# Performance work log

Measured on AMD Instinct MI355X. Metric: run time of the kernel, lower is better.

Reference implementation:

```python
import jax, jax.numpy as jnp
import numpy as np
import math

NUM_BITS = 8
EPS = 1e-5


def fake_quant(x, num_bits=NUM_BITS):
    """Uniform fake quantization over the tensor's full range (min/max), STE-friendly."""
    qmax = 2.0 ** num_bits - 1.0
    mn = jnp.min(x)
    mx = jnp.max(x)
    scale = jnp.maximum((mx - mn) / qmax, 1e-8)
    q = jnp.round(jnp.clip((x - mn) / scale, 0.0, qmax)) * scale + mn
    # straight-through estimator: forward = q, backward = identity
    return x + jax.lax.stop_gradient(q - x)


def qconv(x, w, stride, pad):
    """QConv2d: fake-quantize input (8b) and weight (8b), then fp conv (no bias)."""
    return jax.lax.conv_general_dilated(
        fake_quant(x), fake_quant(w),
        window_strides=(stride, stride),
        padding=[(pad, pad), (pad, pad)],
        dimension_numbers=("NCHW", "OIHW", "NCHW"))


def range_norm(x, gamma, beta):
    """RangeN / RangeBN (Banner et al.): per-channel mean subtraction and
    range-based scale (max-min over N,H,W) with the Gaussian range correction
    factor; affine params with 8-bit fake-quantized gamma."""
    B, C, H, W = x.shape
    n = B * H * W  # elements per channel
    scale_fix = (0.5 * 0.35) * (1.0 + (math.pi * math.log(4.0)) ** 0.5) / ((2.0 * math.log(n)) ** 0.5)
    mean = jnp.mean(x, axis=(0, 2, 3), keepdims=True)          # [1,C,1,1]
    xc = x - mean
    rng = jnp.max(xc, axis=(0, 2, 3), keepdims=True) - jnp.min(xc, axis=(0, 2, 3), keepdims=True)
    out = xc / (rng * scale_fix + EPS)
    qg = fake_quant(gamma)
    return out * qg[None, :, None, None] + beta[None, :, None, None]


def qsum(a, b):
    """Qsum: fake-quantize both addends to 8 bits, then add."""
    return fake_quant(a) + fake_quant(b)


def setup_inputs() -> dict:
    key = jax.random.key(0)
    ks = jax.random.split(key, 4)
    B, Cin, H, W = 64, 1024, 14, 14
    P = 256  # planes; expansion 4 -> Cout = 1024 == Cin (identity residual)
    x = jax.random.normal(ks[0], (B, Cin, H, W), jnp.float32)
    w1 = jax.random.normal(ks[1], (P, Cin, 1, 1), jnp.float32) * (1.0 / math.sqrt(Cin))
    w2 = jax.random.normal(ks[2], (P, P, 3, 3), jnp.float32) * (1.0 / math.sqrt(P * 9))
    w3 = jax.random.normal(ks[3], (4 * P, P, 1, 1), jnp.float32) * (1.0 / math.sqrt(P))
    g1 = jnp.ones((P,), jnp.float32); b1 = jnp.zeros((P,), jnp.float32)
    g2 = jnp.ones((P,), jnp.float32); b2 = jnp.zeros((P,), jnp.float32)
    g3 = jnp.ones((4 * P,), jnp.float32); b3 = jnp.zeros((4 * P,), jnp.float32)
    return {"x": x, "w1": w1, "g1": g1, "b1": b1, "w2": w2, "g2": g2, "b2": b2,
            "w3": w3, "g3": g3, "b3": b3}


def reference(x, w1, g1, b1, w2, g2, b2, w3, g3, b3):
    out = qconv(x, w1, stride=1, pad=0)
    out = range_norm(out, g1, b1)
    out = qconv(out, w2, stride=1, pad=1)
    out = range_norm(out, g2, b2)
    out = qconv(out, w3, stride=1, pad=0)
    out = range_norm(out, g3, b3)
    return qsum(x, out)  # downsample is None -> identity residual
```

## Files before the change

kernel.cpp:

```cpp
#include <hip/hip_runtime.h>
#include <math.h>

#ifndef M_PI
#define M_PI 3.14159265358979323846
#endif

#define NB   64
#define NCOL 12544

typedef __attribute__((ext_vector_type(4))) int int4v;

static const size_t OF_OUT = 0;
static const size_t OF_XC  = 3211264;
static const size_t OF_Z1P = 6422528;
static const size_t OF_Z2C = 7471104;
static const size_t OF_WQ1 = 8273920;
static const size_t OF_WQ2 = 8339456;
static const size_t OF_WQ3 = 8486912;
static const size_t OF_R1  = 8552448;
static const size_t OF_R2  = 8552704;
static const size_t OF_R3  = 8552960;
static const size_t OF_T2  = 8553984;
static const size_t OF_CX  = 8556032;
static const size_t OF_U2  = 8568576;
static const size_t OF_CZ  = 8597504;
static const size_t OF_SD1 = 8610048;
static const size_t OF_SD2 = 8610560;
static const size_t OF_SD3 = 8611072;
static const size_t OF_MN1 = 8613120;
static const size_t OF_MX1 = 8613376;
static const size_t OF_MN2 = 8613632;
static const size_t OF_MX2 = 8613888;
static const size_t OF_MN3 = 8614144;
static const size_t OF_MX3 = 8615168;
static const size_t OF_PMM = 9061632;
static const size_t OF_ST  = 9068800;

__device__ __forceinline__ float fqv(float v, float mn, float sc) {
    float t = (v - mn) / sc;
    t = fminf(fmaxf(t, 0.0f), 255.0f);
    return rintf(t) * sc + mn;
}
__device__ __forceinline__ float codef(float v, float mn, float sc) {
    float t = (v - mn) / sc;
    t = fminf(fmaxf(t, 0.0f), 255.0f);
    return rintf(t) - 128.0f;
}
__device__ __forceinline__ unsigned short f2bf(float f) { return (unsigned short)(__float_as_uint(f) >> 16); }
__device__ __forceinline__ float bf2f(unsigned short u) { return __uint_as_float(((unsigned)u) << 16); }
__device__ __forceinline__ int pack4(float a, float b, float c, float d) {
    return (int)(unsigned char)(signed char)(int)a | ((int)(unsigned char)(signed char)(int)b << 8) |
           ((int)(unsigned char)(signed char)(int)c << 16) | ((int)(unsigned char)(signed char)(int)d << 24);
}
__device__ __forceinline__ void glds16(const void* g, void* l) {
    __builtin_amdgcn_global_load_lds((const __attribute__((address_space(1))) unsigned int*)g,
                                     (__attribute__((address_space(3))) unsigned int*)l, 16, 0, 0);
}
__device__ __forceinline__ unsigned fkey(float f) {
    unsigned u = __float_as_uint(f);
    return (u & 0x80000000u) ? ~u : (u | 0x80000000u);
}
__device__ __forceinline__ float unfkey(unsigned k) {
    unsigned u = (k & 0x80000000u) ? (k & 0x7FFFFFFFu) : ~k;
    return __uint_as_float(u);
}

__device__ __forceinline__ void blk_minmax(float& mn, float& mx, volatile float* scr) {
    for (int o = 32; o; o >>= 1) {
        mn = fminf(mn, __shfl_down(mn, o, 64));
        mx = fmaxf(mx, __shfl_down(mx, o, 64));
    }
    int lane = threadIdx.x & 63, wv = threadIdx.x >> 6;
    __syncthreads();
    if (lane == 0) { scr[wv] = mn; scr[4 + wv] = mx; }
    __syncthreads();
    mn = fminf(fminf(scr[0], scr[1]), fminf(scr[2], scr[3]));
    mx = fmaxf(fmaxf(scr[4], scr[5]), fmaxf(scr[6], scr[7]));
}

template <int C>
__device__ void stage_params(const float* __restrict__ gamma, const float* __restrict__ beta,
                             const double* __restrict__ sumd, const unsigned* __restrict__ mnk,
                             const unsigned* __restrict__ mxk, float scale_fix,
                             float* lmean, float* lsg, volatile float* scr,
                             float& zmn, float& zsc) {
    int t = threadIdx.x;
    float gmn = INFINITY, gmx = -INFINITY;
    for (int c = t; c < C; c += 256) {
        float g = gamma[c];
        gmn = fminf(gmn, g); gmx = fmaxf(gmx, g);
    }
    blk_minmax(gmn, gmx, scr);
    float gsc = fmaxf((gmx - gmn) / 255.0f, 1e-8f);
    float qmn = INFINITY, qmx = -INFINITY;
    for (int c = t; c < C; c += 256) {
        float mean = (float)sumd[c] / 12544.0f;
        float cmn = unfkey(mnk[c]), cmx = unfkey(mxk[c]);
        float rng = cmx - cmn;
        float qg = fqv(gamma[c], gmn, gsc);
        float s = qg / (rng * scale_fix + 1e-5f);
        if (lmean) { lmean[c] = mean; lsg[c] = s; }
        float b = beta[c];
        float lo = (cmn - mean) * s + b;
        float hi = (cmx - mean) * s + b;
        qmn = fminf(qmn, fminf(lo, hi));
        qmx = fmaxf(qmx, fmaxf(lo, hi));
    }
    blk_minmax(qmn, qmx, scr);
    zmn = qmn;
    zsc = fmaxf((qmx - qmn) / 255.0f, 1e-8f);
}

__global__ __launch_bounds__(256) void k_minmax_all(const float4* __restrict__ x, const float4* __restrict__ w1,
                                                    const float4* __restrict__ w2, const float4* __restrict__ w3,
                                                    float* __restrict__ Pmm, float* __restrict__ Wf) {
    {
        unsigned g = blockIdx.x * 256 + threadIdx.x;
        int* zp = (int*)(Wf + OF_Z1P);
        for (unsigned i = g; i < 1048576u; i += 327680u) zp[i] = 0;
        if (g < 12544u) Wf[OF_CX + g] = 0.0f;
        if (g < 16384u) Wf[OF_U2 + g] = 0.0f;
        if (g < 3072u)  ((int*)(Wf + OF_SD1))[g] = 0;
        if (g < 256u) {
            ((unsigned*)(Wf + OF_MN1))[g] = 0xFF800000u;
            ((unsigned*)(Wf + OF_MX1))[g] = 0x007FFFFFu;
            ((unsigned*)(Wf + OF_MN2))[g] = 0xFF800000u;
            ((unsigned*)(Wf + OF_MX2))[g] = 0x007FFFFFu;
        }
        if (g < 1024u) {
            ((unsigned*)(Wf + OF_MN3))[g] = 0xFF800000u;
            ((unsigned*)(Wf + OF_MX3))[g] = 0x007FFFFFu;
        }
    }
    int b = blockIdx.x;
    const float4* p; int lb, nb, n4, base;
    if (b < 1024)      { p = x;  lb = b;        nb = 1024; n4 = 3211264; base = 0; }
    else if (b < 1088) { p = w1; lb = b - 1024; nb = 64;   n4 = 65536;   base = 2048; }
    else if (b < 1216) { p = w2; lb = b - 1088; nb = 128;  n4 = 147456;  base = 2176; }
    else               { p = w3; lb = b - 1216; nb = 64;   n4 = 65536;   base = 2432; }
    float mn = INFINITY, mx = -INFINITY;
    for (int i = lb * 256 + threadIdx.x; i < n4; i += nb * 256) {
        float4 v = p[i];
        mn = fminf(mn, fminf(fminf(v.x, v.y), fminf(v.z, v.w)));
        mx = fmaxf(mx, fmaxf(fmaxf(v.x, v.y), fmaxf(v.z, v.w)));
    }
    for (int o = 32; o; o >>= 1) {
        mn = fminf(mn, __shfl_down(mn, o, 64));
        mx = fmaxf(mx, __shfl_down(mx, o, 64));
    }
    __shared__ float smn[4], smx[4];
    int lane = threadIdx.x & 63, w = threadIdx.x >> 6;
    if (lane == 0) { smn[w] = mn; smx[w] = mx; }
    __syncthreads();
    if (threadIdx.x == 0) {
        for (int i = 1; i < 4; i++) { mn = fminf(mn, smn[i]); mx = fmaxf(mx, smx[i]); }
        Pmm[base + lb * 2]     = mn;
        Pmm[base + lb * 2 + 1] = mx;
    }
}

__global__ __launch_bounds__(256) void k_fqparams2(const float* __restrict__ Pmm, float* __restrict__ sf) {
    __shared__ float sa[4], sb[4];
    int t = threadIdx.x, lane = t & 63, w = t >> 6;
    const int nbs[4]   = {1024, 64, 128, 64};
    const int bases[4] = {0, 2048, 2176, 2432};
    for (int ten = 0; ten < 4; ten++) {
        float mn = INFINITY, mx = -INFINITY;
        for (int i = t; i < nbs[ten]; i += 256) {
            mn = fminf(mn, Pmm[bases[ten] + 2 * i]);
            mx = fmaxf(mx, Pmm[bases[ten] + 2 * i + 1]);
        }
        for (int o = 32; o; o >>= 1) {
            mn = fminf(mn, __shfl_down(mn, o, 64));
            mx = fmaxf(mx, __shfl_down(mx, o, 64));
        }
        if (lane == 0) { sa[w] = mn; sb[w] = mx; }
        __syncthreads();
        if (t == 0) {
            mn = fminf(fminf(sa[0], sa[1]), fminf(sa[2], sa[3]));
            mx = fmaxf(fmaxf(sb[0], sb[1]), fmaxf(sb[2], sb[3]));
            sf[8 + 3 * ten] = mn;
            sf[9 + 3 * ten] = fmaxf((mx - mn) / 255.0f, 1e-8f);
        }
        __syncthreads();
    }
}

__global__ __launch_bounds__(256) void k_wcode_all(const float* __restrict__ w1, const float* __restrict__ w2,
                                                   const float* __restrict__ w3, const float* __restrict__ sf,
                                                   signed char* __restrict__ wq1, signed char* __restrict__ wq2,
                                                   signed char* __restrict__ wq3,
                                                   float* __restrict__ R1, float* __restrict__ R2,
                                                   float* __restrict__ R3, float* __restrict__ T8) {
    __shared__ float sh[64];
    int b = blockIdx.x, t = threadIdx.x;
    int lane = t & 63, wv = t >> 6;
    if (b < 1280) {
        const float* w; signed char* wc; float* R; int K, co; const float* pw;
        if (b < 256) { w = w1; wc = wq1; R = R1; K = 1024; co = b; pw = sf + 11; }
        else         { w = w3; wc = wq3; R = R3; K = 256;  co = b - 256; pw = sf + 17; }
        float mn = pw[0], s = pw[1];
        float sum = 0.f;
        for (int k0 = t * 4; k0 < K; k0 += 1024) {
            float4 v = *(const float4*)&w[(size_t)co * K + k0];
            float c0 = codef(v.x, mn, s), c1 = codef(v.y, mn, s), c2 = codef(v.z, mn, s), c3 = codef(v.w, mn, s);
            *(int*)&wc[(size_t)co * K + k0] = pack4(c0, c1, c2, c3);
            sum += c0 + c1 + c2 + c3;
        }
        for (int o = 32; o; o >>= 1) sum += __shfl_down(sum, o, 64);
        if (lane == 0) sh[wv] = sum;
        __syncthreads();
        if (t == 0) R[co] = sh[0] + sh[1] + sh[2] + sh[3];
    } else {
        int co = b - 1280, ci = t;
        float mn = sf[14], s = sf[15];
        float tp[9];
#pragma unroll
        for (int p = 0; p < 9; p++) {
            float c = codef(w2[((size_t)co * 256 + ci) * 9 + p], mn, s);
            wq2[(size_t)co * 2304 + p * 256 + ci] = (signed char)(int)c;
            tp[p] = c;
        }
        float* red = sh;
        float* sT = sh + 40;
#pragma unroll
        for (int p = 0; p < 9; p++) {
            float v = tp[p];
            for (int o = 32; o; o >>= 1) v += __shfl_down(v, o, 64);
            if (lane == 0) red[wv * 9 + p] = v;
        }
        __syncthreads();
        if (ci < 9) sT[ci] = red[ci] + red[9 + ci] + red[18 + ci] + red[27 + ci];
        __syncthreads();
        if (ci == 0) {
            float T0 = sT[0], T1 = sT[1], T2 = sT[2], T3 = sT[3],
                  T5 = sT[5], T6 = sT[6], T7 = sT[7], T8v = sT[8];
            R2[co] = T0 + T1 + T2 + T3 + sT[4] + T5 + T6 + T7 + T8v;
            float* o = &T8[co * 8];
            o[0] = T0 + T1 + T2;
            o[1] = T6 + T7 + T8v;
            o[2] = T0 + T3 + T6;
            o[3] = T2 + T5 + T8v;
            o[4] = T0; o[5] = T2; o[6] = T6; o[7] = T8v;
        }
    }
}

__global__ __launch_bounds__(256) void k_code0(const float* __restrict__ x, signed char* __restrict__ dst,
                                               const float* __restrict__ qp, float* __restrict__ CX) {
    __shared__ unsigned short lt[28][264];
    int n = blockIdx.z, hw0 = blockIdx.x * 28, cq = blockIdx.y * 256;
    int t = threadIdx.x;
    float qmn = qp[0], qsc = qp[1];
    const float* sp = x + ((size_t)n * 1024 + cq) * 196 + hw0;
    for (int i = t; i < 7168; i += 256) {
        int c = i / 28, hw = i - c * 28;
        lt[hw][c] = f2bf(codef(sp[(size_t)c * 196 + hw], qmn, qsc));
    }
    __syncthreads();
    int lane = t & 63, wv = t >> 6;
    int c0 = lane * 4;
#pragma unroll
    for (int s = 0; s < 7; s++) {
        int i = s * 4 + wv;
        int pk = pack4(bf2f(lt[i][c0]), bf2f(lt[i][c0 + 1]), bf2f(lt[i][c0 + 2]), bf2f(lt[i][c0 + 3]));
        *(int*)&dst[((size_t)n * 196 + hw0 + i) * 1024 + cq + c0] = pk;
    }
    for (int i = wv; i < 28; i += 4) {
        float s = bf2f(lt[i][lane]) + bf2f(lt[i][lane + 64]) +
                  bf2f(lt[i][lane + 128]) + bf2f(lt[i][lane + 192]);
        for (int o = 32; o; o >>= 1) s += __shfl_down(s, o, 64);
        if (lane == 0) atomicAdd(&CX[n * 196 + hw0 + i], s);
    }
}

template <int PAD>
__global__ __launch_bounds__(256) void k_codeE(const float* __restrict__ src, signed char* __restrict__ dst,
                                               const float* __restrict__ gamma, const float* __restrict__ beta_g,
                                               const double* __restrict__ sumd, const unsigned* __restrict__ mnk,
                                               const unsigned* __restrict__ mxk, float scale_fix,
                                               float* __restrict__ rowsum) {
    __shared__ __align__(16) float lmean[256];
    __shared__ __align__(16) float lsg[256];
    __shared__ float scr[8];
    float qmn, qsc;
    stage_params<256>(gamma, beta_g, sumd, mnk, mxk, scale_fix, lmean, lsg, scr, qmn, qsc);
    __syncthreads();
    int t = threadIdx.x, lane = t & 63, wv = t >> 6;
    int c4 = lane * 4;
    float4 m4 = *(const float4*)&lmean[c4];
    float4 s4 = *(const float4*)&lsg[c4];
    float4 b4 = *(const float4*)&beta_g[c4];
#pragma unroll
    for (int r = 0; r < 4; r++) {
        int j = blockIdx.x * 16 + wv * 4 + r;
        float4 v = *(const float4*)&src[(size_t)j * 256 + c4];
        float c0 = codef((v.x - m4.x) * s4.x + b4.x, qmn, qsc);
        float c1 = codef((v.y - m4.y) * s4.y + b4.y, qmn, qsc);
        float c2 = codef((v.z - m4.z) * s4.z + b4.z, qmn, qsc);
        float c3 = codef((v.w - m4.w) * s4.w + b4.w, qmn, qsc);
        int n = j / 196, hw = j - n * 196, h = hw / 14, w = hw - (hw / 14) * 14;
        size_t di;
        if (PAD) di = (((size_t)n * 16 + h + 1) * 16 + (w + 1)) * 256 + c4;
        else     di = (size_t)j * 256 + c4;
        *(int*)&dst[di] = pack4(c0, c1, c2, c3);
        float s = c0 + c1 + c2 + c3;
        for (int o = 32; o; o >>= 1) s += __shfl_down(s, o, 64);
        if (lane == 0) {
            if (PAD) rowsum[((size_t)n * 16 + h + 1) * 16 + (w + 1)] = s;
            else     rowsum[j] = s;
        }
    }
}

template <int MODE>
__global__ __launch_bounds__(256, 2) void k_conv12(const signed char* __restrict__ Acts,
                                                   const signed char* __restrict__ Wts,
                                                   const float* __restrict__ R, const float* __restrict__ T8,
                                                   const float* __restrict__ Cj,
                                                   const float* __restrict__ pw, const float* __restrict__ pz,
                                                   const float* __restrict__ pzg, const float* __restrict__ pzb,
                                                   const double* __restrict__ pzsum,
                                                   const unsigned* __restrict__ pzmn,
                                                   const unsigned* __restrict__ pzmx, float scale_fix,
                                                   float* __restrict__ outNHWC, int K,
                                                   double* __restrict__ Sumd, unsigned* __restrict__ Mnk,
                                                   unsigned* __restrict__ Mxk) {
    __shared__ __align__(16) signed char As[2 * 16384];
    __shared__ __align__(16) signed char Bs[2 * 8192];
    __shared__ float Lst[2][64][3];
    __shared__ float pscr[8];
    int tid = threadIdx.x, lane = tid & 63, wave = tid >> 6;
    int wm = wave >> 1, wn = wave & 1;
    int bid = blockIdx.x;
    int xcd = bid & 7, slot = bid >> 3;
    int tile = xcd * 49 + slot;
    int jb = (tile >> 2) * 128, cob = (tile & 3) * 64;
    int sr = tid >> 3, spos = tid & 7, sc = spos ^ (sr & 7);

    const signed char* aq[4];
#pragma unroll
    for (int q = 0; q < 4; q++) {
        int j = jb + q * 32 + sr;
        if (MODE == 0) aq[q] = Acts + (size_t)j * K + sc * 16;
        else {
            int n = j / 196, hw = j - n * 196, h = hw / 14, w = hw - (hw / 14) * 14;
            aq[q] = Acts + (((size_t)n * 16 + h) * 16 + w) * 256 + sc * 16;
        }
    }
    const signed char* bq[2];
#pragma unroll
    for (int q = 0; q < 2; q++) bq[q] = Wts + (size_t)(cob + q * 32 + sr) * K + sc * 16;

    int nk = K >> 7;
    auto stage = [&](int b, int ks) {
        size_t koA;
        if (MODE == 0) koA = (size_t)ks << 7;
        else {
            int k = ks << 7;
            int p = k >> 8, kin = k & 255;
            int rr = p / 3, ss = p - 3 * rr;
            koA = (size_t)(rr * 16 + ss) * 256 + kin;
        }
#pragma unroll
        for (int q = 0; q < 4; q++)
            glds16(aq[q] + koA, &As[b * 16384 + (q * 32 + sr) * 128 + spos * 16]);
#pragma unroll
        for (int q = 0; q < 2; q++)
            glds16(bq[q] + ((size_t)ks << 7), &Bs[b * 8192 + (q * 32 + sr) * 128 + spos * 16]);
    };

    stage(0, 0);
    float zmn = 0.f, zsc = 0.f;
    if (MODE == 1)
        stage_params<256>(pzg, pzb, pzsum, pzmn, pzmx, scale_fix, nullptr, nullptr, pscr, zmn, zsc);

    int4v acc[4][2];
#pragma unroll
    for (int mi = 0; mi < 4; mi++)
#pragma unroll
        for (int ni = 0; ni < 2; ni++) acc[mi][ni] = (int4v)0;

    int l15 = lane & 15, kq = lane >> 4, sw = l15 & 7;
    for (int ks = 0; ks < nk; ks++) {
        __syncthreads();
        if (ks + 1 < nk) stage((ks + 1) & 1, ks + 1);
        int b = ks & 1;
#pragma unroll
        for (int kc = 0; kc < 2; kc++) {
            int col = ((kc * 4 + kq) ^ sw) << 4;
            int4v a[4], bb[2];
#pragma unroll
            for (int mi = 0; mi < 4; mi++)
                a[mi] = *(const int4v*)&As[b * 16384 + (wm * 64 + mi * 16 + l15) * 128 + col];
#pragma unroll
            for (int ni = 0; ni < 2; ni++)
                bb[ni] = *(const int4v*)&Bs[b * 8192 + (wn * 32 + ni * 16 + l15) * 128 + col];
#pragma unroll
            for (int mi = 0; mi < 4; mi++)
#pragma unroll
                for (int ni = 0; ni < 2; ni++)
                    acc[mi][ni] = __builtin_amdgcn_mfma_i32_16x16x64_i8(a[mi], bb[ni], acc[mi][ni], 0, 0, 0);
        }
    }

    float aw = pw[1], bw = pw[0] + 128.f * pw[1];
    float az, bz;
    if (MODE == 1) { az = zsc; bz = zmn + 128.f * zsc; }
    else           { az = pz[1]; bz = pz[0] + 128.f * pz[1]; }
    float caa = aw * az, cR = aw * bz, cC = bw * az, cK = bw * bz;
    int cco[2]; float rr0[2]; float t8v[2][8];
#pragma unroll
    for (int ni = 0; ni < 2; ni++) {
        cco[ni] = cob + wn * 32 + ni * 16 + l15;
        rr0[ni] = R[cco[ni]];
        if (MODE == 1) {
#pragma unroll
            for (int p = 0; p < 8; p++) t8v[ni][p] = T8[cco[ni] * 8 + p];
        }
    }
    float ssm[2] = {0.f, 0.f}, smnv[2] = {INFINITY, INFINITY}, smxv[2] = {-INFINITY, -INFINITY};
#pragma unroll
    for (int mi = 0; mi < 4; mi++)
#pragma unroll
        for (int reg = 0; reg < 4; reg++) {
            int j = jb + wm * 64 + mi * 16 + kq * 4 + reg;
            int n = j / 196, hw = j - n * 196;
            float constterm, cjv;
            float pt = 0.f, pb = 0.f, pl = 0.f, pr = 0.f, ctl = 0.f, ctr = 0.f, cbl = 0.f, cbr = 0.f;
            if (MODE == 1) {
                int h = hw / 14, w = hw - (hw / 14) * 14;
                pt = (h == 0) ? 1.f : 0.f;  pb = (h == 13) ? 1.f : 0.f;
                pl = (w == 0) ? 1.f : 0.f;  pr = (w == 13) ? 1.f : 0.f;
                ctl = pt * pl; ctr = pt * pr; cbl = pb * pl; cbr = pb * pr;
                float miss = 3.f * (pt + pb + pl + pr) - (ctl + ctr + cbl + cbr);
                constterm = cK * (256.f * (9.f - miss));
                const float* u = Cj + n * 256 + h * 16 + w;
                cjv = u[0] + u[1] + u[2] + u[16] + u[17] + u[18] + u[32] + u[33] + u[34];
            } else {
                constterm = cK * (float)K;
                cjv = Cj[j];
            }
#pragma unroll
            for (int ni = 0; ni < 2; ni++) {
                float rsum = rr0[ni];
                if (MODE == 1)
                    rsum -= pt * t8v[ni][0] + pb * t8v[ni][1] + pl * t8v[ni][2] + pr * t8v[ni][3]
                          - ctl * t8v[ni][4] - ctr * t8v[ni][5] - cbl * t8v[ni][6] - cbr * t8v[ni][7];
                float v = caa * (float)acc[mi][ni][reg] + cR * rsum + cC * cjv + constterm;
                outNHWC[(size_t)j * 256 + cco[ni]] = v;
                ssm[ni] += v;
                smnv[ni] = fminf(smnv[ni], v);
                smxv[ni] = fmaxf(smxv[ni], v);
            }
        }
#pragma unroll
    for (int ni = 0; ni < 2; ni++) {
        float s = ssm[ni], mn = smnv[ni], mx = smxv[ni];
        s += __shfl_xor(s, 16, 64); s += __shfl_xor(s, 32, 64);
        mn = fminf(mn, __shfl_xor(mn, 16, 64)); mn = fminf(mn, __shfl_xor(mn, 32, 64));
        mx = fmaxf(mx, __shfl_xor(mx, 16, 64)); mx = fmaxf(mx, __shfl_xor(mx, 32, 64));
        if (kq == 0) {
            int cl = wn * 32 + ni * 16 + l15;
            Lst[wm][cl][0] = s; Lst[wm][cl][1] = mn; Lst[wm][cl][2] = mx;
        }
    }
    __syncthreads();
    if (tid < 64) {
        float s  = Lst[0][tid][0] + Lst[1][tid][0];
        float mn = fminf(Lst[0][tid][1], Lst[1][tid][1]);
        float mx = fmaxf(Lst[0][tid][2], Lst[1][tid][2]);
        int co = cob + tid;
        atomicAdd(&Sumd[co], (double)s);
        atomicMin(&Mnk[co], fkey(mn));
        atomicMax(&Mxk[co], fkey(mx));
    }
}

__global__ __launch_bounds__(256, 2) void k_conv3(const signed char* __restrict__ Wts,
                                                  const signed char* __restrict__ Zc,
                                                  const float* __restrict__ R, const float* __restrict__ Cj,
                                                  const float* __restrict__ pw,
                                                  const float* __restrict__ pzg, const float* __restrict__ pzb,
                                                  const double* __restrict__ pzsum,
                                                  const unsigned* __restrict__ pzmn,
                                                  const unsigned* __restrict__ pzmx, float scale_fix,
                                                  float* __restrict__ out,
                                                  double* __restrict__ Sumd, unsigned* __restrict__ Mnk,
                                                  unsigned* __restrict__ Mxk) {
    __shared__ __align__(16) signed char As[32768];
    __shared__ __align__(16) signed char Bs[32768];
    __shared__ float Lst[2][128][3];
    __shared__ float pscr[8];
    int tid = threadIdx.x, lane = tid & 63, wave = tid >> 6;
    int wm = wave >> 1, wn = wave & 1;
    int bid = blockIdx.x;
    int xcd = bid & 7, slot = bid >> 3;
    int tile = xcd * 98 + slot;
    int jb = (tile >> 3) * 128, cob = (tile & 7) * 128;
    int sr = tid >> 4, spos = tid & 15;

#pragma unroll
    for (int p = 0; p < 8; p++) {
        int row = p * 16 + sr;
        int cg = spos ^ (row & 7);
        glds16(Zc + (size_t)(jb + row) * 256 + cg * 16, &As[p * 4096 + tid * 16]);
    }
#pragma unroll
    for (int p = 0; p < 8; p++) {
        int row = p * 16 + sr;
        int cg = spos ^ (row & 7);
        glds16(Wts + (size_t)(cob + row) * 256 + cg * 16, &Bs[p * 4096 + tid * 16]);
    }

    float zmn, zsc;
    stage_params<256>(pzg, pzb, pzsum, pzmn, pzmx, scale_fix, nullptr, nullptr, pscr, zmn, zsc);
    __syncthreads();

    int4v acc[4][4];
#pragma unroll
    for (int mi = 0; mi < 4; mi++)
#pragma unroll
        for (int ni = 0; ni < 4; ni++) acc[mi][ni] = (int4v)0;

    int l15 = lane & 15, kq = lane >> 4, sw = l15 & 7;
#pragma unroll
    for (int kc = 0; kc < 4; kc++) {
        int col = ((kc * 4 + kq) ^ sw) << 4;
        int4v a[4], bb[4];
#pragma unroll
        for (int mi = 0; mi < 4; mi++)
            a[mi] = *(const int4v*)&As[(wm * 64 + mi * 16 + l15) * 256 + col];
#pragma unroll
        for (int ni = 0; ni < 4; ni++)
            bb[ni] = *(const int4v*)&Bs[(wn * 64 + ni * 16 + l15) * 256 + col];
#pragma unroll
        for (int mi = 0; mi < 4; mi++)
#pragma unroll
            for (int ni = 0; ni < 4; ni++)
                acc[mi][ni] = __builtin_amdgcn_mfma_i32_16x16x64_i8(a[mi], bb[ni], acc[mi][ni], 0, 0, 0);
    }

    float aw = pw[1], bw = pw[0] + 128.f * pw[1];
    float az = zsc, bz = zmn + 128.f * zsc;
    float caa = aw * az, cR = aw * bz, cC = bw * az, cK = bw * bz;
    int coA[4]; float rA[4];
#pragma unroll
    for (int ni = 0; ni < 4; ni++) {
        coA[ni] = cob + wn * 64 + ni * 16 + l15;
        rA[ni] = R[coA[ni]];
    }
    float ps[4], pmn[4], pmx[4];
#pragma unroll
    for (int ni = 0; ni < 4; ni++) { ps[ni] = 0.f; pmn[ni] = INFINITY; pmx[ni] = -INFINITY; }
#pragma unroll
    for (int mi = 0; mi < 4; mi++) {
        int j0 = jb + wm * 64 + mi * 16 + kq * 4;
        int n = j0 / 196, hh = j0 - n * 196;
        float4 cj = *(const float4*)&Cj[j0];
#pragma unroll
        for (int ni = 0; ni < 4; ni++) {
            float base = cR * rA[ni] + cK * 256.f;
            float4 v;
            v.x = caa * (float)acc[mi][ni][0] + base + cC * cj.x;
            v.y = caa * (float)acc[mi][ni][1] + base + cC * cj.y;
            v.z = caa * (float)acc[mi][ni][2] + base + cC * cj.z;
            v.w = caa * (float)acc[mi][ni][3] + base + cC * cj.w;
            *(float4*)&out[((size_t)n * 1024 + coA[ni]) * 196 + hh] = v;
            ps[ni] += v.x + v.y + v.z + v.w;
            pmn[ni] = fminf(pmn[ni], fminf(fminf(v.x, v.y), fminf(v.z, v.w)));
            pmx[ni] = fmaxf(pmx[ni], fmaxf(fmaxf(v.x, v.y), fmaxf(v.z, v.w)));
        }
    }
#pragma unroll
    for (int ni = 0; ni < 4; ni++) {
        float s = ps[ni], mn = pmn[ni], mx = pmx[ni];
        s += __shfl_xor(s, 16, 64); s += __shfl_xor(s, 32, 64);
        mn = fminf(mn, __shfl_xor(mn, 16, 64)); mn = fminf(mn, __shfl_xor(mn, 32, 64));
        mx = fmaxf(mx, __shfl_xor(mx, 16, 64)); mx = fmaxf(mx, __shfl_xor(mx, 32, 64));
        if (kq == 0) {
            int cl = wn * 64 + ni * 16 + l15;
            Lst[wm][cl][0] = s; Lst[wm][cl][1] = mn; Lst[wm][cl][2] = mx;
        }
    }
    __syncthreads();
    if (tid < 128) {
        float s  = Lst[0][tid][0] + Lst[1][tid][0];
        float mn = fminf(Lst[0][tid][1], Lst[1][tid][1]);
        float mx = fmaxf(Lst[0][tid][2], Lst[1][tid][2]);
        int co = cob + tid;
        atomicAdd(&Sumd[co], (double)s);
        atomicMin(&Mnk[co], fkey(mn));
        atomicMax(&Mxk[co], fkey(mx));
    }
}

__global__ __launch_bounds__(256) void k_final(const float* __restrict__ x, float* __restrict__ out,
                                               const float* __restrict__ gamma, const float* __restrict__ beta,
                                               const double* __restrict__ sumd, const unsigned* __restrict__ mnk,
                                               const unsigned* __restrict__ mxk, float scale_fix,
                                               const float* __restrict__ sf) {
    __shared__ float lmean[1024];
    __shared__ float lsg[1024];
    __shared__ float scr[8];
    float qmn, qsc;
    stage_params<1024>(gamma, beta, sumd, mnk, mxk, scale_fix, lmean, lsg, scr, qmn, qsc);
    __syncthreads();
    float xmn = sf[8], xsc = sf[9];
    const float4* xp = (const float4*)x;
    float4* yp = (float4*)out;
    int n4 = 12845056 / 4;
    int i = blockIdx.x * blockDim.x + threadIdx.x;
    int str = gridDim.x * blockDim.x;
    for (; i < n4; i += str) {
        int e = i * 4;
        int c = (e / 196) & 1023;
        float m = lmean[c], s = lsg[c], b = beta[c];
        float4 xv = xp[i], ov = yp[i], r;
        r.x = fqv(xv.x, xmn, xsc) + fqv((ov.x - m) * s + b, qmn, qsc);
        r.y = fqv(xv.y, xmn, xsc) + fqv((ov.y - m) * s + b, qmn, qsc);
        r.z = fqv(xv.z, xmn, xsc) + fqv((ov.z - m) * s + b, qmn, qsc);
        r.w = fqv(xv.w, xmn, xsc) + fqv((ov.w - m) * s + b, qmn, qsc);
        yp[i] = r;
    }
}

extern "C" void kernel_launch(void* const* d_in, const int* in_sizes, int n_in,
                              void* d_out, int out_size, void* d_ws, size_t ws_size,
                              hipStream_t stream) {
    const float* x  = (const float*)d_in[0];
    const float* w1 = (const float*)d_in[1];
    const float* g1 = (const float*)d_in[2];
    const float* b1 = (const float*)d_in[3];
    const float* w2 = (const float*)d_in[4];
    const float* g2 = (const float*)d_in[5];
    const float* b2 = (const float*)d_in[6];
    const float* w3 = (const float*)d_in[7];
    const float* g3 = (const float*)d_in[8];
    const float* b3 = (const float*)d_in[9];
    float* out = (float*)d_out;

    float* W = (float*)d_ws;
    float* OUT = W + OF_OUT;
    signed char* xc  = (signed char*)(W + OF_XC);
    signed char* z1p = (signed char*)(W + OF_Z1P);
    signed char* z2c = (signed char*)(W + OF_Z2C);
    signed char* wq1 = (signed char*)(W + OF_WQ1);
    signed char* wq2 = (signed char*)(W + OF_WQ2);
    signed char* wq3 = (signed char*)(W + OF_WQ3);
    float* R1 = W + OF_R1; float* R2 = W + OF_R2; float* R3 = W + OF_R3;
    float* T2 = W + OF_T2;
    float* CX = W + OF_CX; float* U2 = W + OF_U2; float* CZ = W + OF_CZ;
    double* SD1 = (double*)(W + OF_SD1);
    double* SD2 = (double*)(W + OF_SD2);
    double* SD3 = (double*)(W + OF_SD3);
    unsigned* MN1 = (unsigned*)(W + OF_MN1); unsigned* MX1 = (unsigned*)(W + OF_MX1);
    unsigned* MN2 = (unsigned*)(W + OF_MN2); unsigned* MX2 = (unsigned*)(W + OF_MX2);
    unsigned* MN3 = (unsigned*)(W + OF_MN3); unsigned* MX3 = (unsigned*)(W + OF_MX3);
    float* Pmm = W + OF_PMM;
    float* S = W + OF_ST;

    const float scale_fix =
        (float)((0.5 * 0.35) * (1.0 + sqrt(M_PI * log(4.0))) / sqrt(2.0 * log(12544.0)));

    k_minmax_all<<<1280, 256, 0, stream>>>((const float4*)x, (const float4*)w1,
                                           (const float4*)w2, (const float4*)w3, Pmm, W);
    k_fqparams2<<<1, 256, 0, stream>>>(Pmm, S);

    k_wcode_all<<<1536, 256, 0, stream>>>(w1, w2, w3, S, wq1, wq2, wq3, R1, R2, R3, T2);

    k_code0<<<dim3(7, 4, 64), 256, 0, stream>>>(x, xc, S + 8, CX);

    k_conv12<0><<<392, 256, 0, stream>>>(xc, wq1, R1, nullptr, CX, S + 11, S + 8,
                                         nullptr, nullptr, nullptr, nullptr, nullptr, 0.f,
                                         OUT, 1024, SD1, MN1, MX1);
    k_codeE<1><<<784, 256, 0, stream>>>(OUT, z1p, g1, b1, SD1, MN1, MX1, scale_fix, U2);

    k_conv12<1><<<392, 256, 0, stream>>>(z1p, wq2, R2, T2, U2, S + 14, nullptr,
                                         g1, b1, SD1, MN1, MX1, scale_fix,
                                         OUT, 2304, SD2, MN2, MX2);
    k_codeE<0><<<784, 256, 0, stream>>>(OUT, z2c, g2, b2, SD2, MN2, MX2, scale_fix, CZ);

    k_conv3<<<784, 256, 0, stream>>>(wq3, z2c, R3, CZ, S + 17,
                                     g2, b2, SD2, MN2, MX2, scale_fix,
                                     out, SD3, MN3, MX3);

    k_final<<<2048, 256, 0, stream>>>(x, out, g3, b3, SD3, MN3, MX3, scale_fix, S);
}
```

Before: 247.1 us.

## Merge prep kernels, reuse int8 input codes in final residual, precompute conv2 column sums

The activation coding kernel and the weight coding kernel are merged into one launch, which removes a kernel boundary. The final residual kernel now reads the int8 quantized input codes (NHWC), staged into LDS through direct global-to-LDS loads, instead of rereading the fp32 input. This cuts that read traffic to a quarter. The kernel is regridded to one block per (batch, 128-channel) slice. Conv2 precomputes its per-column 3x3 neighbourhood sums into shared memory once per block rather than in the epilogue. The cost is a larger LDS footprint in the final kernel and fewer blocks (512), which may lower occupancy.

```diff
diff --git a/kernel.cpp b/kernel.cpp
--- a/kernel.cpp
+++ b/kernel.cpp
@@ -186,15 +186,45 @@
     }
 }
 
-__global__ __launch_bounds__(256) void k_wcode_all(const float* __restrict__ w1, const float* __restrict__ w2,
-                                                   const float* __restrict__ w3, const float* __restrict__ sf,
-                                                   signed char* __restrict__ wq1, signed char* __restrict__ wq2,
-                                                   signed char* __restrict__ wq3,
-                                                   float* __restrict__ R1, float* __restrict__ R2,
-                                                   float* __restrict__ R3, float* __restrict__ T8) {
+__global__ __launch_bounds__(256) void k_prep(const float* __restrict__ x, signed char* __restrict__ xdst,
+                                              const float* __restrict__ sf, float* __restrict__ CX,
+                                              const float* __restrict__ w1, const float* __restrict__ w2,
+                                              const float* __restrict__ w3,
+                                              signed char* __restrict__ wq1, signed char* __restrict__ wq2,
+                                              signed char* __restrict__ wq3,
+                                              float* __restrict__ R1, float* __restrict__ R2,
+                                              float* __restrict__ R3, float* __restrict__ T8) {
+    int t = threadIdx.x;
+    int lane = t & 63, wv = t >> 6;
+    if (blockIdx.x < 1792) {
+        __shared__ unsigned short lt[28][264];
+        int u = blockIdx.x;
+        int n = u / 28, r = u - n * 28;
+        int hw0 = (r % 7) * 28, cq = (r / 7) * 256;
+        float qmn = sf[8], qsc = sf[9];
+        const float* sp = x + ((size_t)n * 1024 + cq) * 196 + hw0;
+        for (int i = t; i < 7168; i += 256) {
+            int c = i / 28, hw = i - c * 28;
+            lt[hw][c] = f2bf(codef(sp[(size_t)c * 196 + hw], qmn, qsc));
+        }
+        __syncthreads();
+        int c0 = lane * 4;
+#pragma unroll
+        for (int s = 0; s < 7; s++) {
+            int i = s * 4 + wv;
+            int pk = pack4(bf2f(lt[i][c0]), bf2f(lt[i][c0 + 1]), bf2f(lt[i][c0 + 2]), bf2f(lt[i][c0 + 3]));
+            *(int*)&xdst[((size_t)n * 196 + hw0 + i) * 1024 + cq + c0] = pk;
+        }
+        for (int i = wv; i < 28; i += 4) {
+            float s = bf2f(lt[i][lane]) + bf2f(lt[i][lane + 64]) +
+                      bf2f(lt[i][lane + 128]) + bf2f(lt[i][lane + 192]);
+            for (int o = 32; o; o >>= 1) s += __shfl_down(s, o, 64);
+            if (lane == 0) atomicAdd(&CX[n * 196 + hw0 + i], s);
+        }
+        return;
+    }
     __shared__ float sh[64];
-    int b = blockIdx.x, t = threadIdx.x;
-    int lane = t & 63, wv = t >> 6;
+    int b = blockIdx.x - 1792;
     if (b < 1280) {
         const float* w; signed char* wc; float* R; int K, co; const float* pw;
         if (b < 256) { w = w1; wc = wq1; R = R1; K = 1024; co = b; pw = sf + 11; }
@@ -243,34 +273,6 @@
             o[3] = T2 + T5 + T8v;
             o[4] = T0; o[5] = T2; o[6] = T6; o[7] = T8v;
         }
-    }
-}
-
-__global__ __launch_bounds__(256) void k_code0(const float* __restrict__ x, signed char* __restrict__ dst,
-                                               const float* __restrict__ qp, float* __restrict__ CX) {
-    __shared__ unsigned short lt[28][264];
-    int n = blockIdx.z, hw0 = blockIdx.x * 28, cq = blockIdx.y * 256;
-    int t = threadIdx.x;
-    float qmn = qp[0], qsc = qp[1];
-    const float* sp = x + ((size_t)n * 1024 + cq) * 196 + hw0;
-    for (int i = t; i < 7168; i += 256) {
-        int c = i / 28, hw = i - c * 28;
-        lt[hw][c] = f2bf(codef(sp[(size_t)c * 196 + hw], qmn, qsc));
-    }
-    __syncthreads();
-    int lane = t & 63, wv = t >> 6;
-    int c0 = lane * 4;
-#pragma unroll
-    for (int s = 0; s < 7; s++) {
-        int i = s * 4 + wv;
-        int pk = pack4(bf2f(lt[i][c0]), bf2f(lt[i][c0 + 1]), bf2f(lt[i][c0 + 2]), bf2f(lt[i][c0 + 3]));
-        *(int*)&dst[((size_t)n * 196 + hw0 + i) * 1024 + cq + c0] = pk;
-    }
-    for (int i = wv; i < 28; i += 4) {
-        float s = bf2f(lt[i][lane]) + bf2f(lt[i][lane + 64]) +
-                  bf2f(lt[i][lane + 128]) + bf2f(lt[i][lane + 192]);
-        for (int o = 32; o; o >>= 1) s += __shfl_down(s, o, 64);
-        if (lane == 0) atomicAdd(&CX[n * 196 + hw0 + i], s);
     }
 }
 
@@ -330,6 +332,7 @@
     __shared__ __align__(16) signed char Bs[2 * 8192];
     __shared__ float Lst[2][64][3];
     __shared__ float pscr[8];
+    __shared__ float Vl[128];
     int tid = threadIdx.x, lane = tid & 63, wave = tid >> 6;
     int wm = wave >> 1, wn = wave & 1;
     int bid = blockIdx.x;
@@ -372,8 +375,15 @@
 
     stage(0, 0);
     float zmn = 0.f, zsc = 0.f;
-    if (MODE == 1)
+    if (MODE == 1) {
         stage_params<256>(pzg, pzb, pzsum, pzmn, pzmx, scale_fix, nullptr, nullptr, pscr, zmn, zsc);
+        if (tid < 128) {
+            int j = jb + tid;
+            int n_ = j / 196, hw_ = j - n_ * 196, h_ = hw_ / 14, w_ = hw_ - (hw_ / 14) * 14;
+            const float* u = Cj + n_ * 256 + h_ * 16 + w_;
+            Vl[tid] = u[0] + u[1] + u[2] + u[16] + u[17] + u[18] + u[32] + u[33] + u[34];
+        }
+    }
 
     int4v acc[4][2];
 #pragma unroll
@@ -435,8 +445,7 @@
                 ctl = pt * pl; ctr = pt * pr; cbl = pb * pl; cbr = pb * pr;
                 float miss = 3.f * (pt + pb + pl + pr) - (ctl + ctr + cbl + cbr);
                 constterm = cK * (256.f * (9.f - miss));
-                const float* u = Cj + n * 256 + h * 16 + w;
-                cjv = u[0] + u[1] + u[2] + u[16] + u[17] + u[18] + u[32] + u[33] + u[34];
+                cjv = Vl[j - jb];
             } else {
                 constterm = cK * (float)K;
                 cjv = Cj[j];
@@ -595,33 +604,47 @@
     }
 }
 
-__global__ __launch_bounds__(256) void k_final(const float* __restrict__ x, float* __restrict__ out,
+__global__ __launch_bounds__(256) void k_final(const signed char* __restrict__ xc, float* __restrict__ out,
                                                const float* __restrict__ gamma, const float* __restrict__ beta,
                                                const double* __restrict__ sumd, const unsigned* __restrict__ mnk,
                                                const unsigned* __restrict__ mxk, float scale_fix,
                                                const float* __restrict__ sf) {
+    __shared__ __align__(16) signed char lx[196 * 128];
     __shared__ float lmean[1024];
     __shared__ float lsg[1024];
     __shared__ float scr[8];
+    int t = threadIdx.x;
+    int n = blockIdx.x >> 3, cq = blockIdx.x & 7;
+    const signed char* src = xc + (size_t)n * 196 * 1024 + cq * 128;
+    for (int ch = t; ch < 1568; ch += 256) {
+        int hw = ch >> 3, col = ch & 7;
+        glds16(src + (size_t)hw * 1024 + col * 16, &lx[ch * 16]);
+    }
     float qmn, qsc;
     stage_params<1024>(gamma, beta, sumd, mnk, mxk, scale_fix, lmean, lsg, scr, qmn, qsc);
+    float xmn = sf[8], xsc = sf[9];
+    float xoff = xmn + 128.f * xsc;
+    asm volatile("s_waitcnt vmcnt(0)" ::: "memory");
     __syncthreads();
-    float xmn = sf[8], xsc = sf[9];
-    const float4* xp = (const float4*)x;
-    float4* yp = (float4*)out;
-    int n4 = 12845056 / 4;
-    int i = blockIdx.x * blockDim.x + threadIdx.x;
-    int str = gridDim.x * blockDim.x;
-    for (; i < n4; i += str) {
-        int e = i * 4;
-        int c = (e / 196) & 1023;
-        float m = lmean[c], s = lsg[c], b = beta[c];
-        float4 xv = xp[i], ov = yp[i], r;
-        r.x = fqv(xv.x, xmn, xsc) + fqv((ov.x - m) * s + b, qmn, qsc);
-        r.y = fqv(xv.y, xmn, xsc) + fqv((ov.y - m) * s + b, qmn, qsc);
-        r.z = fqv(xv.z, xmn, xsc) + fqv((ov.z - m) * s + b, qmn, qsc);
-        r.w = fqv(xv.w, xmn, xsc) + fqv((ov.w - m) * s + b, qmn, qsc);
-        yp[i] = r;
+    int cl = t & 127;
+    int c = cq * 128 + cl;
+    float m = lmean[c], s = lsg[c], b = beta[c];
+    float4* rowp = (float4*)(out + ((size_t)n * 1024 + c) * 196);
+    int f0 = (t < 128) ? 0 : 25;
+    int f1 = (t < 128) ? 25 : 49;
+    for (int f = f0; f < f1; f++) {
+        float4 ov = rowp[f];
+        int hw = f * 4;
+        float x0 = (float)lx[(hw + 0) * 128 + cl] * xsc + xoff;
+        float x1 = (float)lx[(hw + 1) * 128 + cl] * xsc + xoff;
+        float x2 = (float)lx[(hw + 2) * 128 + cl] * xsc + xoff;
+        float x3 = (float)lx[(hw + 3) * 128 + cl] * xsc + xoff;
+        float4 r;
+        r.x = x0 + fqv((ov.x - m) * s + b, qmn, qsc);
+        r.y = x1 + fqv((ov.y - m) * s + b, qmn, qsc);
+        r.z = x2 + fqv((ov.z - m) * s + b, qmn, qsc);
+        r.w = x3 + fqv((ov.w - m) * s + b, qmn, qsc);
+        rowp[f] = r;
     }
 }
 
@@ -667,9 +690,7 @@
                                            (const float4*)w2, (const float4*)w3, Pmm, W);
     k_fqparams2<<<1, 256, 0, stream>>>(Pmm, S);
 
-    k_wcode_all<<<1536, 256, 0, stream>>>(w1, w2, w3, S, wq1, wq2, wq3, R1, R2, R3, T2);
-
-    k_code0<<<dim3(7, 4, 64), 256, 0, stream>>>(x, xc, S + 8, CX);
+    k_prep<<<3328, 256, 0, stream>>>(x, xc, S, CX, w1, w2, w3, wq1, wq2, wq3, R1, R2, R3, T2);
 
     k_conv12<0><<<392, 256, 0, stream>>>(xc, wq1, R1, nullptr, CX, S + 11, S + 8,
                                          nullptr, nullptr, nullptr, nullptr, nullptr, 0.f,
@@ -685,5 +706,5 @@
                                      g2, b2, SD2, MN2, MX2, scale_fix,
                                      out, SD3, MN3, MX3);
 
-    k_final<<<2048, 256, 0, stream>>>(x, out, g3, b3, SD3, MN3, MX3, scale_fix, S);
-}
+    k_final<<<512, 256, 0, stream>>>(xc, out, g3, b3, SD3, MN3, MX3, scale_fix, S);
+}
```

After: 254.8 us. 1.03x slower.
